# Kernel optimization log

Measured on AMD Instinct MI355X. Metric: run time of the kernel, lower is better.

The kernel has to match this reference:

```python
import jax, jax.numpy as jnp
import numpy as np

B, T, C, U, W = 8, 2048, 512, 512, 2


def setup_inputs() -> dict:
    key = jax.random.key(0)
    k1, k2 = jax.random.split(key)
    x = jax.random.normal(k1, (B, T, C), dtype=jnp.float32)
    # Conv1D kernel: [window, in_channels, 3*units] (z, f, o gates), glorot-ish scale
    kernel = jax.random.normal(k2, (W, C, 3 * U), dtype=jnp.float32) * (1.0 / np.sqrt(W * C))
    bias = jnp.zeros((3 * U,), dtype=jnp.float32)
    initial_state = jnp.zeros((1, U), dtype=jnp.float32)
    return {"x": x, "kernel": kernel, "bias": bias, "initial_state": initial_state}


def reference(x, kernel, bias, initial_state):
    # Causal Conv1D: pad (window-1) on the left of the time axis.
    window = kernel.shape[0]
    gates = jax.lax.conv_general_dilated(
        x, kernel,
        window_strides=(1,),
        padding=[(window - 1, 0)],
        dimension_numbers=("NWC", "WIO", "NWC"),
    ) + bias  # [B, T, 3U]
    z, f, o = jnp.split(gates, 3, axis=-1)
    z = jnp.tanh(z)
    f = jax.nn.sigmoid(f)
    o = jax.nn.sigmoid(o)

    # fo-pool recurrence: h_t = f_t * h_{t-1} + (1 - f_t) * z_t
    h0 = jnp.repeat(initial_state, x.shape[0], axis=0)  # [B, U]
    fs = jnp.moveaxis(f, 1, 0)  # [T, B, U]
    zs = jnp.moveaxis(z, 1, 0)  # [T, B, U]

    def step(h, fz):
        f_t, z_t = fz
        h = f_t * h + (1.0 - f_t) * z_t
        return h, h

    _, hs = jax.lax.scan(step, h0, (fs, zs))  # hs: [T, B, U]
    recurrent = jnp.moveaxis(hs, 0, 1)  # [B, T, U]

    # output gate, return_sequences=True
    return recurrent * o
```

## Files before the change

### kernel.cpp

```cpp
#include <hip/hip_runtime.h>


#define Bn 8
#define Tn 2048
#define Cn 512
#define Un 512
#define Nn 1536
#define Kn 1024
#define Mn (Bn * Tn)
#define NC 32
#define CL 64

using bf16x8 = __attribute__((ext_vector_type(8))) __bf16;
using f32x4  = __attribute__((ext_vector_type(4))) float;

__device__ __forceinline__ void async16(const void* g, void* l) {
  __builtin_amdgcn_global_load_lds((const __attribute__((address_space(1))) void*)g,
                                   (__attribute__((address_space(3))) void*)l, 16, 0, 0);
}

__device__ __forceinline__ unsigned short f2bf(float v) {
  union { float f; unsigned u; } c; c.f = v;
  unsigned u = c.u;
  return (unsigned short)((u + 0x7fffu + ((u >> 16) & 1u)) >> 16);
}

__device__ __forceinline__ float bf2f(unsigned short h) {
  union { unsigned u; float f; } c; c.u = ((unsigned)h) << 16;
  return c.f;
}

__device__ __forceinline__ float fast_sigmoid(float x) {
  float e = __builtin_amdgcn_exp2f(-1.4426950408889634f * x);
  return __builtin_amdgcn_rcpf(1.0f + e);
}
__device__ __forceinline__ float fast_tanh(float x) {
  float e = __builtin_amdgcn_exp2f(-2.8853900817779268f * x);
  return 2.0f * __builtin_amdgcn_rcpf(1.0f + e) - 1.0f;
}

__global__ __launch_bounds__(256) void conv_x(const float* __restrict__ x,
                                              unsigned short* __restrict__ xb) {
  int idx = blockIdx.x * 256 + threadIdx.x;
  int c4  = idx & 127;
  int row = idx >> 7;
  int b   = row / (Tn + 1);
  int t   = row - b * (Tn + 1);
  ushort4 ov;
  if (t == 0) {
    ov.x = ov.y = ov.z = ov.w = 0;
  } else {
    float4 v = *(const float4*)(x + (size_t)(b * Tn + t - 1) * Cn + c4 * 4);
    ov.x = f2bf(v.x); ov.y = f2bf(v.y); ov.z = f2bf(v.z); ov.w = f2bf(v.w);
  }
  *(ushort4*)(xb + (size_t)row * Cn + c4 * 4) = ov;
}

__global__ __launch_bounds__(256) void conv_k(const float* __restrict__ kern,
                                              unsigned short* __restrict__ kT) {
  __shared__ float tile[32][33];
  int kb = blockIdx.x, nb = blockIdx.y;
  int tx = threadIdx.x & 31, ty = threadIdx.x >> 5;
#pragma unroll
  for (int i = 0; i < 4; i++)
    tile[ty + i * 8][tx] = kern[(size_t)(kb * 32 + ty + i * 8) * Nn + nb * 32 + tx];
  __syncthreads();
#pragma unroll
  for (int i = 0; i < 4; i++) {
    int n = nb * 32 + ty + i * 8;
    int k = kb * 32 + tx;
    kT[(size_t)n * Kn + k] = f2bf(tile[tx][ty + i * 8]);
  }
}

__global__ __launch_bounds__(256) void gemm_gates(const unsigned short* __restrict__ xb,
                                                  const unsigned short* __restrict__ kT,
                                                  const float* __restrict__ bias,
                                                  unsigned short* __restrict__ gates) {
  __shared__ unsigned short As[128 * 64];
  __shared__ unsigned short Bs[128 * 64];
  const int tid = threadIdx.x;
  const int m0 = blockIdx.x * 128;
  const int n0 = blockIdx.y * 128;
  const int batch = m0 / Tn;
  const int lane = tid & 63;
  const int w = tid >> 6, wr = w >> 1, wc = w & 1;

  const int srow = (w << 3) + (lane >> 3);
  const int skq  = (lane & 7) ^ (lane >> 3);
  const unsigned short* aStage = xb + (size_t)(m0 + batch + srow) * Cn + (skq << 3);
  const unsigned short* bStage = kT + (size_t)(n0 + srow) * Kn + (skq << 3);

  f32x4 zero = {0.f, 0.f, 0.f, 0.f};
  f32x4 acc[4][4];
#pragma unroll
  for (int i = 0; i < 4; i++)
#pragma unroll
    for (int j = 0; j < 4; j++) acc[i][j] = zero;

  const int rA0 = wr * 64 + (lane & 15);
  const int rB0 = wc * 64 + (lane & 15);
  const int swz = lane & 7;

  for (int k0 = 0; k0 < Kn; k0 += 64) {
#pragma unroll
    for (int j = 0; j < 4; j++) {
      async16(aStage + (size_t)(j << 5) * Cn + k0, &As[(j * 256 + tid) * 8]);
      async16(bStage + (size_t)(j << 5) * Kn + k0, &Bs[(j * 256 + tid) * 8]);
    }
    __builtin_amdgcn_s_waitcnt(0);
    __syncthreads();

#pragma unroll
    for (int ks = 0; ks < 2; ks++) {
      const int col = (((ks << 2) + (lane >> 4)) ^ swz) << 3;
      bf16x8 af[4], bf[4];
#pragma unroll
      for (int i = 0; i < 4; i++) {
        af[i] = *(const bf16x8*)&As[(rA0 + i * 16) * 64 + col];
        bf[i] = *(const bf16x8*)&Bs[(rB0 + i * 16) * 64 + col];
      }
#pragma unroll
      for (int i = 0; i < 4; i++)
#pragma unroll
        for (int j = 0; j < 4; j++)
          acc[i][j] = __builtin_amdgcn_mfma_f32_16x16x32_bf16(af[i], bf[j], acc[i][j], 0, 0, 0);
    }
    __syncthreads();
  }

  const int region = blockIdx.y >> 2;
  const int rowB = wr * 64 + (lane >> 4) * 4;
  const int colB = wc * 64 + (lane & 15);
#pragma unroll
  for (int i = 0; i < 4; i++)
#pragma unroll
    for (int j = 0; j < 4; j++)
#pragma unroll
      for (int r = 0; r < 4; r++) {
        int mm = m0 + rowB + i * 16 + r;
        int nn = n0 + colB + j * 16;
        float g = acc[i][j][r] + bias[nn];
        float a = (region == 0) ? fast_tanh(g) : fast_sigmoid(g);
        gates[(size_t)mm * Nn + nn] = f2bf(a);
      }
}

__global__ __launch_bounds__(256) void scan_phaseA(const unsigned short* __restrict__ gates,
                                                   float* __restrict__ aArr,
                                                   float* __restrict__ bArr) {
  int chunk = blockIdx.x >> 1;
  int u = (blockIdx.x & 1) * 256 + threadIdx.x;
  int b = chunk >> 5, c = chunk & (NC - 1);
  const unsigned short* gp = gates + (size_t)(b * Tn + c * CL) * Nn;
  float a = 1.0f, bv = 0.0f;
#pragma unroll 4
  for (int t = 0; t < CL; t++) {
    float z = bf2f(gp[u]);
    float f = bf2f(gp[Un + u]);
    a *= f;
    bv = f * bv + (1.0f - f) * z;
    gp += Nn;
  }
  aArr[(size_t)chunk * Un + u] = a;
  bArr[(size_t)chunk * Un + u] = bv;
}

__global__ __launch_bounds__(256) void scan_phaseB(const float* __restrict__ aArr,
                                                   const float* __restrict__ bArr,
                                                   const float* __restrict__ init,
                                                   float* __restrict__ hstart) {
  int idx = blockIdx.x * 256 + threadIdx.x;
  int b = idx >> 9, u = idx & (Un - 1);
  float h = init[u];
  for (int c = 0; c < NC; c++) {
    size_t offc = (size_t)(b * NC + c) * Un + u;
    hstart[offc] = h;
    h = aArr[offc] * h + bArr[offc];
  }
}

__global__ __launch_bounds__(256) void scan_phaseC(const unsigned short* __restrict__ gates,
                                                   const float* __restrict__ hstart,
                                                   float* __restrict__ out) {
  int chunk = blockIdx.x >> 1;
  int u = (blockIdx.x & 1) * 256 + threadIdx.x;
  int b = chunk >> 5, c = chunk & (NC - 1);
  const unsigned short* gp = gates + (size_t)(b * Tn + c * CL) * Nn;
  float* op = out + (size_t)(b * Tn + c * CL) * Un;
  float h = hstart[(size_t)chunk * Un + u];
#pragma unroll 4
  for (int t = 0; t < CL; t++) {
    float z = bf2f(gp[u]);
    float f = bf2f(gp[Un + u]);
    float o = bf2f(gp[2 * Un + u]);
    h = f * h + (1.0f - f) * z;
    op[u] = h * o;
    gp += Nn;
    op += Un;
  }
}

extern "C" void kernel_launch(void* const* d_in, const int* in_sizes, int n_in,
                              void* d_out, int out_size, void* d_ws, size_t ws_size,
                              hipStream_t stream) {
  const float* x    = (const float*)d_in[0];
  const float* kern = (const float*)d_in[1];
  const float* bias = (const float*)d_in[2];
  const float* init = (const float*)d_in[3];
  float* out = (float*)d_out;

  char* ws = (char*)d_ws;
  unsigned short* xb = (unsigned short*)ws;
  size_t off = (size_t)Bn * (Tn + 1) * Cn * 2;
  unsigned short* kT = (unsigned short*)(ws + off);
  off += (size_t)Nn * Kn * 2;
  unsigned short* gates = (unsigned short*)(ws + off);
  off += (size_t)Mn * Nn * 2;
  float* aArr = (float*)(ws + off);  off += (size_t)Bn * NC * Un * 4;
  float* bArr = (float*)(ws + off);  off += (size_t)Bn * NC * Un * 4;
  float* hstart = (float*)(ws + off);

  conv_x<<<(Bn * (Tn + 1) * Cn / 4) / 256, 256, 0, stream>>>(x, xb);
  conv_k<<<dim3(32, 48), 256, 0, stream>>>(kern, kT);
  gemm_gates<<<dim3(Mn / 128, Nn / 128), 256, 0, stream>>>(xb, kT, bias, gates);
  scan_phaseA<<<Bn * NC * 2, 256, 0, stream>>>(gates, aArr, bArr);
  scan_phaseB<<<(Bn * Un) / 256, 256, 0, stream>>>(aArr, bArr, init, hstart);
  scan_phaseC<<<Bn * NC * 2, 256, 0, stream>>>(gates, hstart, out);
}
```

Before: 175.8 us.

## Fuse scan carry propagation into phase C and vectorize gate loads

```diff
diff --git a/kernel.cpp b/kernel.cpp
--- a/kernel.cpp
+++ b/kernel.cpp
@@ -13,6 +13,7 @@
 
 using bf16x8 = __attribute__((ext_vector_type(8))) __bf16;
 using f32x4  = __attribute__((ext_vector_type(4))) float;
+using us8    = __attribute__((ext_vector_type(8))) unsigned short;
 
 __device__ __forceinline__ void async16(const void* g, void* l) {
   __builtin_amdgcn_global_load_lds((const __attribute__((address_space(1))) void*)g,
@@ -24,11 +25,11 @@
   unsigned u = c.u;
   return (unsigned short)((u + 0x7fffu + ((u >> 16) & 1u)) >> 16);
 }
-
-__device__ __forceinline__ float bf2f(unsigned short h) {
-  union { unsigned u; float f; } c; c.u = ((unsigned)h) << 16;
-  return c.f;
-}
+__device__ __forceinline__ float asf(unsigned u) {
+  union { unsigned u; float f; } c; c.u = u; return c.f;
+}
+__device__ __forceinline__ float bf_lo(unsigned w) { return asf(w << 16); }
+__device__ __forceinline__ float bf_hi(unsigned w) { return asf(w & 0xffff0000u); }
 
 __device__ __forceinline__ float fast_sigmoid(float x) {
   float e = __builtin_amdgcn_exp2f(-1.4426950408889634f * x);
@@ -42,18 +43,21 @@
 __global__ __launch_bounds__(256) void conv_x(const float* __restrict__ x,
                                               unsigned short* __restrict__ xb) {
   int idx = blockIdx.x * 256 + threadIdx.x;
-  int c4  = idx & 127;
-  int row = idx >> 7;
+  int c8  = idx & 63;
+  int row = idx >> 6;
   int b   = row / (Tn + 1);
   int t   = row - b * (Tn + 1);
-  ushort4 ov;
+  us8 ov;
   if (t == 0) {
-    ov.x = ov.y = ov.z = ov.w = 0;
+    ov = (us8)0;
   } else {
-    float4 v = *(const float4*)(x + (size_t)(b * Tn + t - 1) * Cn + c4 * 4);
-    ov.x = f2bf(v.x); ov.y = f2bf(v.y); ov.z = f2bf(v.z); ov.w = f2bf(v.w);
-  }
-  *(ushort4*)(xb + (size_t)row * Cn + c4 * 4) = ov;
+    const float* src = x + (size_t)(b * Tn + t - 1) * Cn + c8 * 8;
+    float4 v0 = *(const float4*)src;
+    float4 v1 = *(const float4*)(src + 4);
+    ov[0] = f2bf(v0.x); ov[1] = f2bf(v0.y); ov[2] = f2bf(v0.z); ov[3] = f2bf(v0.w);
+    ov[4] = f2bf(v1.x); ov[5] = f2bf(v1.y); ov[6] = f2bf(v1.z); ov[7] = f2bf(v1.w);
+  }
+  *(us8*)(xb + (size_t)row * Cn + c8 * 8) = ov;
 }
 
 __global__ __launch_bounds__(256) void conv_k(const float* __restrict__ kern,
@@ -147,55 +151,56 @@
 }
 
 __global__ __launch_bounds__(256) void scan_phaseA(const unsigned short* __restrict__ gates,
-                                                   float* __restrict__ aArr,
-                                                   float* __restrict__ bArr) {
-  int chunk = blockIdx.x >> 1;
-  int u = (blockIdx.x & 1) * 256 + threadIdx.x;
+                                                   unsigned int* __restrict__ ab) {
+  int chunk = blockIdx.x;
   int b = chunk >> 5, c = chunk & (NC - 1);
+  int u2 = threadIdx.x * 2;
   const unsigned short* gp = gates + (size_t)(b * Tn + c * CL) * Nn;
-  float a = 1.0f, bv = 0.0f;
-#pragma unroll 4
+  float a0 = 1.f, a1 = 1.f, bv0 = 0.f, bv1 = 0.f;
+#pragma unroll 8
   for (int t = 0; t < CL; t++) {
-    float z = bf2f(gp[u]);
-    float f = bf2f(gp[Un + u]);
-    a *= f;
-    bv = f * bv + (1.0f - f) * z;
+    unsigned zz = *(const unsigned*)(gp + u2);
+    unsigned ff = *(const unsigned*)(gp + Un + u2);
+    float z0 = bf_lo(zz), z1 = bf_hi(zz);
+    float f0 = bf_lo(ff), f1 = bf_hi(ff);
+    a0 *= f0; a1 *= f1;
+    bv0 = f0 * bv0 + (1.0f - f0) * z0;
+    bv1 = f1 * bv1 + (1.0f - f1) * z1;
     gp += Nn;
   }
-  aArr[(size_t)chunk * Un + u] = a;
-  bArr[(size_t)chunk * Un + u] = bv;
-}
-
-__global__ __launch_bounds__(256) void scan_phaseB(const float* __restrict__ aArr,
-                                                   const float* __restrict__ bArr,
+  uint2 w;
+  w.x = ((unsigned)f2bf(a0) << 16) | f2bf(bv0);
+  w.y = ((unsigned)f2bf(a1) << 16) | f2bf(bv1);
+  *(uint2*)(ab + (size_t)chunk * Un + u2) = w;
+}
+
+__global__ __launch_bounds__(256) void scan_phaseC(const unsigned short* __restrict__ gates,
+                                                   const unsigned int* __restrict__ ab,
                                                    const float* __restrict__ init,
-                                                   float* __restrict__ hstart) {
-  int idx = blockIdx.x * 256 + threadIdx.x;
-  int b = idx >> 9, u = idx & (Un - 1);
-  float h = init[u];
-  for (int c = 0; c < NC; c++) {
-    size_t offc = (size_t)(b * NC + c) * Un + u;
-    hstart[offc] = h;
-    h = aArr[offc] * h + bArr[offc];
-  }
-}
-
-__global__ __launch_bounds__(256) void scan_phaseC(const unsigned short* __restrict__ gates,
-                                                   const float* __restrict__ hstart,
                                                    float* __restrict__ out) {
-  int chunk = blockIdx.x >> 1;
-  int u = (blockIdx.x & 1) * 256 + threadIdx.x;
+  int chunk = blockIdx.x;
   int b = chunk >> 5, c = chunk & (NC - 1);
+  int u2 = threadIdx.x * 2;
+  float h0 = init[u2], h1 = init[u2 + 1];
+  for (int cp = 0; cp < c; cp++) {
+    uint2 w = *(const uint2*)(ab + (size_t)(b * NC + cp) * Un + u2);
+    h0 = asf(w.x & 0xffff0000u) * h0 + bf_lo(w.x);
+    h1 = asf(w.y & 0xffff0000u) * h1 + bf_lo(w.y);
+  }
   const unsigned short* gp = gates + (size_t)(b * Tn + c * CL) * Nn;
   float* op = out + (size_t)(b * Tn + c * CL) * Un;
-  float h = hstart[(size_t)chunk * Un + u];
-#pragma unroll 4
+#pragma unroll 8
   for (int t = 0; t < CL; t++) {
-    float z = bf2f(gp[u]);
-    float f = bf2f(gp[Un + u]);
-    float o = bf2f(gp[2 * Un + u]);
-    h = f * h + (1.0f - f) * z;
-    op[u] = h * o;
+    unsigned zz = *(const unsigned*)(gp + u2);
+    unsigned ff = *(const unsigned*)(gp + Un + u2);
+    unsigned oo = *(const unsigned*)(gp + 2 * Un + u2);
+    float z0 = bf_lo(zz), z1 = bf_hi(zz);
+    float f0 = bf_lo(ff), f1 = bf_hi(ff);
+    float o0 = bf_lo(oo), o1 = bf_hi(oo);
+    h0 = f0 * h0 + (1.0f - f0) * z0;
+    h1 = f1 * h1 + (1.0f - f1) * z1;
+    float2 ov; ov.x = h0 * o0; ov.y = h1 * o1;
+    *(float2*)(op + u2) = ov;
     gp += Nn;
     op += Un;
   }
@@ -217,14 +222,11 @@
   off += (size_t)Nn * Kn * 2;
   unsigned short* gates = (unsigned short*)(ws + off);
   off += (size_t)Mn * Nn * 2;
-  float* aArr = (float*)(ws + off);  off += (size_t)Bn * NC * Un * 4;
-  float* bArr = (float*)(ws + off);  off += (size_t)Bn * NC * Un * 4;
-  float* hstart = (float*)(ws + off);
-
-  conv_x<<<(Bn * (Tn + 1) * Cn / 4) / 256, 256, 0, stream>>>(x, xb);
+  unsigned int* ab = (unsigned int*)(ws + off);
+
+  conv_x<<<(Bn * (Tn + 1) * Cn / 8) / 256, 256, 0, stream>>>(x, xb);
   conv_k<<<dim3(32, 48), 256, 0, stream>>>(kern, kT);
   gemm_gates<<<dim3(Mn / 128, Nn / 128), 256, 0, stream>>>(xb, kT, bias, gates);
-  scan_phaseA<<<Bn * NC * 2, 256, 0, stream>>>(gates, aArr, bArr);
-  scan_phaseB<<<(Bn * Un) / 256, 256, 0, stream>>>(aArr, bArr, init, hstart);
-  scan_phaseC<<<Bn * NC * 2, 256, 0, stream>>>(gates, hstart, out);
-}
+  scan_phaseA<<<Bn * NC, 256, 0, stream>>>(gates, ab);
+  scan_phaseC<<<Bn * NC, 256, 0, stream>>>(gates, ab, init, out);
+}
```

Result: no change. 178.1 us (+1.3%).
